# Kernel tuning notes

Hardware: AMD Instinct MI355X
Metric: run time of the kernel (lower is better)

Reference implementation:

```python
import math
import jax, jax.numpy as jnp
import numpy as np

B, S, D = 8, 512, 1024        # batch, seq (dec and enc), model dim
HID, NH = 1024, 16            # attention hidden, heads
C = HID // NH                 # per-head channels (self-attn 'attends' over this dim!)
EPS = 1e-5


def setup_inputs() -> dict:
    key = jax.random.key(0)
    ks = jax.random.split(key, 26)
    w = lambda k, sh: (jax.random.normal(k, sh, jnp.float32) * 0.02)
    inp = {
        "x": jax.random.normal(ks[0], (B, S, D), jnp.float32),
        "h": jax.random.normal(ks[1], (B, S, D), jnp.float32),
        # self-attn (AttentionModule) params, stored [in, out]
        "Wq": w(ks[2], (D, HID)), "bq": jnp.zeros((HID,), jnp.float32),
        "Wk": w(ks[3], (D, HID)), "bk": jnp.zeros((HID,), jnp.float32),
        "Wv": w(ks[4], (D, HID)), "bv": jnp.zeros((HID,), jnp.float32),
        "Wo": w(ks[5], (HID, D)), "bo": jnp.zeros((D,), jnp.float32),
        # cross-attn params
        "Wcq": w(ks[6], (D, HID)), "bcq": jnp.zeros((HID,), jnp.float32),
        "Wck": w(ks[7], (D, HID)), "bck": jnp.zeros((HID,), jnp.float32),
        "Wcv": w(ks[8], (D, HID)), "bcv": jnp.zeros((HID,), jnp.float32),
        "Wco": w(ks[9], (HID, D)), "bco": jnp.zeros((D,), jnp.float32),
        "gamma": jnp.ones((D,), jnp.float32), "beta": jnp.zeros((D,), jnp.float32),
        # FFN (two Linears, NO nonlinearity, per original code)
        "W1": w(ks[10], (D, HID)), "b1": jnp.zeros((HID,), jnp.float32),
        "W2": w(ks[11], (HID, D)), "b2": jnp.zeros((D,), jnp.float32),
    }
    return inp


def _layernorm(x, gamma, beta):
    mu = jnp.mean(x, axis=-1, keepdims=True)
    var = jnp.mean(jnp.square(x - mu), axis=-1, keepdims=True)
    return (x - mu) * jax.lax.rsqrt(var + EPS) * gamma + beta


def _self_attn(x, Wq, bq, Wk, bk, Wv, bv, Wo, bo):
    # FAITHFUL to original: reshape [B,S,NH,C]; einsum '...hq,...hk->...hqk' with
    # batch dims [B,S] -> attention over the C channel dim per token, causal mask over channels.
    Q = (x @ Wq + bq).reshape(B, S, NH, C) / math.sqrt(C)
    K = (x @ Wk + bk).reshape(B, S, NH, C)
    V = (x @ Wv + bv).reshape(B, S, NH, C)
    aff = jnp.einsum('bshq,bshk->bshqk', Q, K)            # [B,S,NH,C,C]
    mask = jnp.triu(jnp.full((C, C), -jnp.inf, jnp.float32), k=1)  # -inf above diag, 0 else
    aff = aff + mask
    w = jax.nn.softmax(aff, axis=-1)
    av = jnp.einsum('bshqk,bshk->bshq', w, V)             # [B,S,NH,C]
    return av.reshape(B, S, HID) @ Wo + bo


def _cross_attn(xd, he, Wcq, bcq, Wck, bck, Wcv, bcv, Wco, bco):
    # standard multi-head cross attention, but scaled by sqrt(d_full) per original
    Q = (xd @ Wcq + bcq).reshape(B, S, NH, C).transpose(0, 2, 1, 3)  # [B,NH,Sq,C]
    K = (he @ Wck + bck).reshape(B, S, NH, C).transpose(0, 2, 1, 3)
    V = (he @ Wcv + bcv).reshape(B, S, NH, C).transpose(0, 2, 1, 3)
    scores = jnp.einsum('bhqd,bhkd->bhqk', Q, K) / math.sqrt(HID)
    p = jax.nn.softmax(scores, axis=-1)
    o = jnp.einsum('bhqk,bhkd->bhqd', p, V)               # [B,NH,Sq,C]
    o = o.transpose(0, 2, 1, 3).reshape(B, S, HID)
    return o @ Wco + bco


def reference(x, h, Wq, bq, Wk, bk, Wv, bv, Wo, bo,
              Wcq, bcq, Wck, bck, Wcv, bcv, Wco, bco,
              gamma, beta, W1, b1, W2, b2):
    out = _self_attn(x, Wq, bq, Wk, bk, Wv, bv, Wo, bo) + x
    out = _layernorm(out, gamma, beta)
    out = _cross_attn(out, h, Wcq, bcq, Wck, bck, Wcv, bcv, Wco, bco) + out
    out = _layernorm(out, gamma, beta)
    out = ((out @ W1 + b1) @ W2 + b2) + out
    out = _layernorm(out, gamma, beta)
    return out
```

## Files before the change

### kernel.cpp

```cpp
#include <hip/hip_runtime.h>

typedef __bf16 bf16_t;
typedef bf16_t bf16x8 __attribute__((ext_vector_type(8)));
typedef bf16_t bf16x4 __attribute__((ext_vector_type(4)));
typedef float f32x4 __attribute__((ext_vector_type(4)));
typedef unsigned u32x4 __attribute__((ext_vector_type(4)));

__device__ __forceinline__ void async_copy16(const void* g, void* l) {
  __builtin_amdgcn_global_load_lds(
      (const __attribute__((address_space(1))) unsigned int*)(unsigned long long)g,
      (__attribute__((address_space(3))) unsigned int*)(unsigned int)(unsigned long long)l,
      16, 0, 0);
}

__device__ __forceinline__ float fast_exp2(float x) {
#if __has_builtin(__builtin_amdgcn_exp2f)
  return __builtin_amdgcn_exp2f(x);
#else
  float r;
  asm volatile("v_exp_f32 %0, %1\n\ts_nop 0" : "=v"(r) : "v"(x));
  return r;
#endif
}
__device__ __forceinline__ float fast_rcp(float x) {
#if __has_builtin(__builtin_amdgcn_rcpf)
  return __builtin_amdgcn_rcpf(x);
#else
  float r;
  asm volatile("v_rcp_f32 %0, %1\n\ts_nop 0" : "=v"(r) : "v"(x));
  return r;
#endif
}

__device__ __forceinline__ unsigned pack_bf16(float x, float y) {
  bf16_t lo = (bf16_t)x, hi = (bf16_t)y;
  unsigned short ul, uh;
  __builtin_memcpy(&ul, &lo, 2);
  __builtin_memcpy(&uh, &hi, 2);
  return (unsigned)ul | ((unsigned)uh << 16);
}

#define QSCALE 0.180336688f

struct SrcPtrs { const float* p[10]; };
__global__ __launch_bounds__(256) void prep_main(
    SrcPtrs srcs, bf16_t* __restrict__ dstbase,
    const float* __restrict__ a, const float* __restrict__ b,
    const float* __restrict__ w1, bf16_t* __restrict__ dst1,
    bf16_t* __restrict__ dstw) {
  __shared__ float tile[32][33];
  int bid = blockIdx.x;
  int tid = threadIdx.x;
  if (bid < 10240) {
    int z = bid >> 10;
    int rem = bid & 1023;
    const float* src = srcs.p[z];
    bf16_t* dst = dstbase + (size_t)z * 1048576;
    float scale = (z == 0) ? QSCALE : ((z == 4) ? 0.03125f : 1.f);
    int bx = (rem & 31) * 32;
    int by = (rem >> 5) * 32;
    int tx = tid & 31, ty = tid >> 5;
#pragma unroll
    for (int i = 0; i < 32; i += 8)
      tile[ty + i][tx] = src[(size_t)(by + ty + i) * 1024 + bx + tx];
    __syncthreads();
#pragma unroll
    for (int i = 0; i < 32; i += 8)
      dst[(size_t)(bx + ty + i) * 1024 + by + tx] = (bf16_t)(tile[tx][ty + i] * scale);
  } else {
    int i = ((bid - 10240) * 256 + tid) * 8;
    const float* s;
    bf16_t* d;
    if (i < 4194304) { s = a + i; d = dst1 + i; }
    else if (i < 8388608) { s = b + i - 4194304; d = dst1 + i; }
    else { s = w1 + i - 8388608; d = dstw + (i - 8388608); }
    float4 u = *(const float4*)s;
    float4 v = *(const float4*)(s + 4);
    bf16x8 o;
    o[0]=(bf16_t)u.x; o[1]=(bf16_t)u.y; o[2]=(bf16_t)u.z; o[3]=(bf16_t)u.w;
    o[4]=(bf16_t)v.x; o[5]=(bf16_t)v.y; o[6]=(bf16_t)v.z; o[7]=(bf16_t)v.w;
    *(bf16x8*)d = o;
  }
}

__global__ __launch_bounds__(256) void prep_bias_kernel(
    const float* __restrict__ bq, const float* __restrict__ bk,
    const float* __restrict__ bv, const float* __restrict__ bck,
    const float* __restrict__ bcv, const float* __restrict__ bcq,
    const bf16_t* __restrict__ wt9, const float* __restrict__ b1,
    const float* __restrict__ b2, float* __restrict__ cb,
    float* __restrict__ cb2) {
  int bid = blockIdx.x;
  if (bid < 28) {
    int i = bid * 256 + threadIdx.x;
    if (i < 1024) cb[i] = bq[i] * QSCALE;
    else if (i < 2048) cb[i] = bk[i - 1024];
    else if (i < 3072) cb[i] = bv[i - 2048];
    else if (i < 4096) cb[i] = bck[i - 3072];
    else if (i < 5120) cb[i] = bcv[i - 4096];
    else if (i < 6144) cb[i] = bcq[i - 5120] * 0.03125f;
    else cb[i] = 0.f;
  } else {
    int n = (bid - 28) * 256 + threadIdx.x;
    const bf16_t* row = wt9 + (size_t)n * 1024;
    float acc = 0.f;
#pragma unroll 4
    for (int h = 0; h < 1024; h += 8) {
      bf16x8 v = *(const bf16x8*)(row + h);
      float4 ba = *(const float4*)(b1 + h);
      float4 bb = *(const float4*)(b1 + h + 4);
      acc += ba.x*(float)v[0] + ba.y*(float)v[1] + ba.z*(float)v[2] + ba.w*(float)v[3]
           + bb.x*(float)v[4] + bb.y*(float)v[5] + bb.z*(float)v[6] + bb.w*(float)v[7];
    }
    cb2[n] = acc + b2[n];
  }
}

template <int BN, int MI, bool HAS_RES, bool TRANS_OUT, bool DBUF>
__device__ __forceinline__ void gemm_core(
    const bf16_t* __restrict__ A, const bf16_t* __restrict__ Bt,
    const float* __restrict__ bias, const bf16_t* __restrict__ res,
    bf16_t* __restrict__ C, int ldC, int bm, int bn,
    bf16_t* As, bf16_t* Bs) {
  constexpr int NI = 4;
  constexpr int ASZ = 128 * 64, BSZ = BN * 64;
  int tid = threadIdx.x;
  int w = tid >> 6, lane = tid & 63;
  int fm = lane & 15, fq = lane >> 4;
  int wm = (BN == 128) ? (w >> 1) * 64 : w * 32;
  int wn = (BN == 128) ? (w & 1) * 64 : 0;
  f32x4 acc[MI][NI] = {};

  auto stage = [&](int kt, int half) {
    bf16_t* Ad = DBUF ? As + half * ASZ : As;
    bf16_t* Bd = DBUF ? Bs + half * BSZ : Bs;
#pragma unroll
    for (int i = 0; i < 4; i++) {
      int c = i * 256 + tid;
      int row = c >> 3, skg = (c & 7) ^ (row & 7);
      async_copy16(A + (size_t)(bm + row) * 1024 + kt + skg * 8, &Ad[c * 8]);
    }
#pragma unroll
    for (int i = 0; i < BN / 32; i++) {
      int c = i * 256 + tid;
      int row = c >> 3, skg = (c & 7) ^ (row & 7);
      async_copy16(Bt + (size_t)(bn + row) * 1024 + kt + skg * 8, &Bd[c * 8]);
    }
  };
  auto compute = [&](int half) {
    const bf16_t* Ac = DBUF ? As + half * ASZ : As;
    const bf16_t* Bc = DBUF ? Bs + half * BSZ : Bs;
#pragma unroll
    for (int ks = 0; ks < 2; ks++) {
      bf16x8 af[MI], bfr[NI];
      int kg = ks * 4 + fq;
#pragma unroll
      for (int mi = 0; mi < MI; mi++) {
        int row = wm + mi * 16 + fm;
        af[mi] = *(const bf16x8*)&Ac[row * 64 + ((kg ^ (row & 7)) * 8)];
      }
#pragma unroll
      for (int ni = 0; ni < NI; ni++) {
        int row = wn + ni * 16 + fm;
        bfr[ni] = *(const bf16x8*)&Bc[row * 64 + ((kg ^ (row & 7)) * 8)];
      }
#pragma unroll
      for (int mi = 0; mi < MI; mi++)
#pragma unroll
        for (int ni = 0; ni < NI; ni++)
          acc[mi][ni] = __builtin_amdgcn_mfma_f32_16x16x32_bf16(
              af[mi], bfr[ni], acc[mi][ni], 0, 0, 0);
    }
  };

  if (DBUF) {
    stage(0, 0);
    __syncthreads();
#pragma unroll
    for (int t = 0; t < 16; t++) {
      if (t < 15) stage((t + 1) * 64, (t + 1) & 1);
      compute(t & 1);
      __syncthreads();
    }
  } else {
    for (int kt = 0; kt < 1024; kt += 64) {
      stage(kt, 0);
      __syncthreads();
      compute(0);
      __syncthreads();
    }
  }

#pragma unroll
  for (int mi = 0; mi < MI; mi++) {
#pragma unroll
    for (int ni = 0; ni < NI; ni++) {
      int col = bn + wn + ni * 16 + fm;
      float bv = bias[col];
      if (TRANS_OUT) {
        int rowb = bm + wm + mi * 16 + fq * 4;
        bf16x4 w4;
#pragma unroll
        for (int r = 0; r < 4; r++) w4[r] = (bf16_t)(acc[mi][ni][r] + bv);
        *(bf16x4*)&C[(size_t)col * ldC + rowb] = w4;
      } else {
#pragma unroll
        for (int r = 0; r < 4; r++) {
          int row = bm + wm + mi * 16 + fq * 4 + r;
          float v = acc[mi][ni][r] + bv;
          if (HAS_RES) v += (float)res[(size_t)row * ldC + col];
          C[(size_t)row * ldC + col] = (bf16_t)v;
        }
      }
    }
  }
}

template <int GX, int GY, int BN>
__device__ __forceinline__ void xcd_map(int lin, int& bm, int& bn) {
  constexpr int HX = GX / 2, QY = GY / 4;
  int xcd = lin & 7, idx = lin >> 3;
  int ly = idx / HX, lx = idx - ly * HX;
  bm = ((xcd >> 1) * QY + ly) * 128;
  bn = ((xcd & 1) * HX + lx) * BN;
}

template <bool HAS_RES, bool TRANS_OUT>
__global__ __launch_bounds__(256) void gemm_bf16(
    const bf16_t* __restrict__ A, const bf16_t* __restrict__ Bt,
    const float* __restrict__ bias, const bf16_t* __restrict__ res,
    bf16_t* __restrict__ C, int ldC) {
  __shared__ bf16_t As[2 * 128 * 64];
  __shared__ bf16_t Bs[2 * 64 * 64];
  int bm, bn;
  xcd_map<16, 32, 64>(blockIdx.x + 16 * blockIdx.y, bm, bn);
  gemm_core<64, 2, HAS_RES, TRANS_OUT, true>(A, Bt, bias, res, C, ldC, bm, bn, As, Bs);
}

__global__ __launch_bounds__(256) void gemm_qkv_p(
    const bf16_t* __restrict__ xb, const bf16_t* __restrict__ wt0,
    const bf16_t* __restrict__ wt9, const bf16_t* __restrict__ w1bf,
    const float* __restrict__ cb, bf16_t* __restrict__ qkv,
    bf16_t* __restrict__ pt) {
  __shared__ bf16_t smem[2 * 128 * 64];
  int bid = blockIdx.x;
  if (bid >= 128) {
    int bm, bn;
    xcd_map<24, 32, 128>(bid - 128, bm, bn);
    gemm_core<128, 4, false, false, false>(xb, wt0, cb, nullptr, qkv, 3072,
                                           bm, bn, smem, smem + 128 * 64);
  } else {
    gemm_core<64, 2, false, false, false>(wt9, w1bf, cb + 6144, nullptr, pt, 1024,
                                          (bid >> 4) * 128, (bid & 15) * 64,
                                          smem, smem + 128 * 64);
  }
}

__global__ __launch_bounds__(256) void gemm_cqkv(
    const bf16_t* __restrict__ t1n, const bf16_t* __restrict__ hb,
    const bf16_t* __restrict__ wt4, const float* __restrict__ cb,
    bf16_t* __restrict__ cq, bf16_t* __restrict__ kbuf,
    bf16_t* __restrict__ vt) {
  __shared__ bf16_t As[128 * 64];
  __shared__ bf16_t Bs[64 * 64];
  int lin = blockIdx.x + 48 * blockIdx.y;
  int xcd = lin & 7, idx = lin >> 3;
  int ly = idx / 24, lx = idx - ly * 24;
  int bm = ((xcd >> 1) * 8 + ly) * 128;
  int gx = (xcd & 1) * 24 + lx;
  int region = gx >> 4;
  int bn = (gx & 15) * 64;
  const bf16_t* Bt = wt4 + (size_t)region * 1048576;
  if (region == 2) {
    gemm_core<64, 2, false, true, false>(hb, Bt, cb + 4096, nullptr, vt, 4096,
                                         bm, bn, As, Bs);
  } else if (region == 1) {
    gemm_core<64, 2, false, false, false>(hb, Bt, cb + 3072, nullptr, kbuf, 1024,
                                          bm, bn, As, Bs);
  } else {
    gemm_core<64, 2, false, false, false>(t1n, Bt, cb + 5120, nullptr, cq, 1024,
                                          bm, bn, As, Bs);
  }
}

__global__ __launch_bounds__(256) void self_attn_kernel(
    const bf16_t* __restrict__ QKV, bf16_t* __restrict__ O) {
  int tid = threadIdx.x;
  int lane = tid & 63;
  int unit = __builtin_amdgcn_readfirstlane(blockIdx.x * 4 + (tid >> 6));
  int m = unit >> 4, h = unit & 15;
  size_t base = (size_t)m * 3072 + h * 64;
  size_t iq = base + lane;
  float qv = (float)QKV[iq];
  float kown = (float)QKV[iq + 1024];
  float vown = (float)QKV[iq + 2048];
  const u32x4* Krow = (const u32x4*)(QKV + base + 1024);
  const u32x4* Vrow = (const u32x4*)(QKV + base + 2048);
  u32x4 K4[8], V4[8];
#pragma unroll
  for (int i = 0; i < 8; i++) { K4[i] = Krow[i]; V4[i] = Vrow[i]; }
  float l0 = 0.f, l1 = 0.f, o0 = 0.f, o1 = 0.f;
#pragma unroll
  for (int p = 0; p < 32; p++) {
    unsigned kw = K4[p >> 2][p & 3];
    unsigned vw = V4[p >> 2][p & 3];
    float k0 = __uint_as_float(kw << 16);
    float k1 = __uint_as_float(kw & 0xffff0000u);
    float v0 = __uint_as_float(vw << 16);
    float v1 = __uint_as_float(vw & 0xffff0000u);
    float e0 = fast_exp2(qv * k0);
    float e1 = fast_exp2(qv * k1);
    bool c = lane >= 2 * p + 1;
    e0 = c ? e0 : 0.f;
    e1 = c ? e1 : 0.f;
    l0 += e0; o0 = fmaf(e0, v0, o0);
    l1 += e1; o1 = fmaf(e1, v1, o1);
  }
  float ed = fast_exp2(qv * kown);
  ed = ((lane & 1) == 0) ? ed : 0.f;
  float l = (l0 + l1) + ed;
  float o = fmaf(ed, vown, o0 + o1);
  O[(size_t)m * 1024 + h * 64 + lane] = (bf16_t)(o * fast_rcp(l));
}

__global__ __launch_bounds__(256) void cross_attn_mfma(
    const bf16_t* __restrict__ Q, const bf16_t* __restrict__ Kb,
    const bf16_t* __restrict__ Vt, bf16_t* __restrict__ O) {
  __shared__ bf16_t Ks[64 * 64];
  __shared__ bf16_t Vs[64 * 64];
  int tid = threadIdx.x;
  int w = tid >> 6, lane = tid & 63;
  int fm = lane & 15, fq = lane >> 4;
  int bh = blockIdx.x;
  int b = bh >> 4, h = bh & 15;
  int q0 = blockIdx.y * 64 + w * 16;
  const bf16_t* Qp = Q + (size_t)(b * 512 + q0 + fm) * 1024 + h * 64 + fq * 8;
  bf16x8 qf0 = *(const bf16x8*)Qp;
  bf16x8 qf1 = *(const bf16x8*)(Qp + 32);
  f32x4 o[4] = {};
  float mx = -1e30f, l = 0.f;
  for (int k0 = 0; k0 < 512; k0 += 64) {
    __syncthreads();
#pragma unroll
    for (int i = 0; i < 2; i++) {
      int c = i * 256 + tid;
      int row = c >> 3, kg = (c & 7) ^ (row & 7);
      async_copy16(Kb + (size_t)(b * 512 + k0 + row) * 1024 + h * 64 + kg * 8,
                   &Ks[c * 8]);
      async_copy16(Vt + (size_t)(h * 64 + row) * 4096 + b * 512 + k0 + kg * 8,
                   &Vs[c * 8]);
    }
    __syncthreads();
    f32x4 s[4] = {};
#pragma unroll
    for (int mt = 0; mt < 4; mt++) {
      int row = mt * 16 + fm;
#pragma unroll
      for (int f = 0; f < 2; f++) {
        int kg = f * 4 + fq;
        bf16x8 kf = *(const bf16x8*)&Ks[row * 64 + ((kg ^ (row & 7)) * 8)];
        s[mt] = __builtin_amdgcn_mfma_f32_16x16x32_bf16(
            kf, (f ? qf1 : qf0), s[mt], 0, 0, 0);
      }
    }
    float smax = -1e30f;
#pragma unroll
    for (int mt = 0; mt < 4; mt++)
#pragma unroll
      for (int r = 0; r < 4; r++) smax = fmaxf(smax, s[mt][r]);
    smax = fmaxf(smax, __shfl_xor(smax, 16, 64));
    smax = fmaxf(smax, __shfl_xor(smax, 32, 64));
    float nm = fmaxf(mx, smax);
    float corr = __expf(mx - nm);
    float ladd = 0.f;
    unsigned pk0[4], pk1[4];
#pragma unroll
    for (int mt = 0; mt < 4; mt++) {
      float p0 = __expf(s[mt][0] - nm);
      float p1 = __expf(s[mt][1] - nm);
      float p2 = __expf(s[mt][2] - nm);
      float p3 = __expf(s[mt][3] - nm);
      ladd += (p0 + p1) + (p2 + p3);
      pk0[mt] = pack_bf16(p0, p1);
      pk1[mt] = pack_bf16(p2, p3);
    }
    ladd += __shfl_xor(ladd, 16, 64);
    ladd += __shfl_xor(ladd, 32, 64);
    l = l * corr + ladd;
#pragma unroll
    for (int ct = 0; ct < 4; ct++)
#pragma unroll
      for (int r = 0; r < 4; r++) o[ct][r] *= corr;
    union U { unsigned u[4]; bf16x8 v; } pf[2];
    int sl0 = ((fq & 1) * 2) * 16 + fm;
    int sl1 = sl0 + 16;
    bool hi = fq >= 2;
#pragma unroll
    for (int f = 0; f < 2; f++) {
      unsigned a0 = (unsigned)__shfl((int)pk0[f * 2],     sl0, 64);
      unsigned b0 = (unsigned)__shfl((int)pk0[f * 2 + 1], sl0, 64);
      unsigned a1 = (unsigned)__shfl((int)pk1[f * 2],     sl0, 64);
      unsigned b1 = (unsigned)__shfl((int)pk1[f * 2 + 1], sl0, 64);
      unsigned a2 = (unsigned)__shfl((int)pk0[f * 2],     sl1, 64);
      unsigned b2 = (unsigned)__shfl((int)pk0[f * 2 + 1], sl1, 64);
      unsigned a3 = (unsigned)__shfl((int)pk1[f * 2],     sl1, 64);
      unsigned b3 = (unsigned)__shfl((int)pk1[f * 2 + 1], sl1, 64);
      pf[f].u[0] = hi ? b0 : a0;
      pf[f].u[1] = hi ? b1 : a1;
      pf[f].u[2] = hi ? b2 : a2;
      pf[f].u[3] = hi ? b3 : a3;
    }
#pragma unroll
    for (int ct = 0; ct < 4; ct++) {
      int row = ct * 16 + fm;
#pragma unroll
      for (int f = 0; f < 2; f++) {
        int kg = f * 4 + fq;
        bf16x8 vf = *(const bf16x8*)&Vs[row * 64 + ((kg ^ (row & 7)) * 8)];
        o[ct] = __builtin_amdgcn_mfma_f32_16x16x32_bf16(vf, pf[f].v, o[ct], 0, 0, 0);
      }
    }
    mx = nm;
  }
  float inv = 1.f / l;
  bf16_t* Op = O + (size_t)(b * 512 + q0 + fm) * 1024 + h * 64 + fq * 4;
#pragma unroll
  for (int ct = 0; ct < 4; ct++) {
    bf16x4 w4;
    w4[0] = (bf16_t)(o[ct][0] * inv);
    w4[1] = (bf16_t)(o[ct][1] * inv);
    w4[2] = (bf16_t)(o[ct][2] * inv);
    w4[3] = (bf16_t)(o[ct][3] * inv);
    *(bf16x4*)(Op + ct * 16) = w4;
  }
}

template <typename OutT>
__global__ __launch_bounds__(256) void ln_kernel(
    const bf16_t* __restrict__ X, const float* __restrict__ gamma,
    const float* __restrict__ beta, OutT* __restrict__ Y) {
  __shared__ float red[8];
  int row = blockIdx.x;
  int tid = threadIdx.x;
  bf16x4 x4 = *(const bf16x4*)(X + (size_t)row * 1024 + tid * 4);
  float4 v = {(float)x4[0], (float)x4[1], (float)x4[2], (float)x4[3]};
  float s = (v.x + v.y) + (v.z + v.w);
  float ss = fmaf(v.x, v.x, fmaf(v.y, v.y, fmaf(v.z, v.z, v.w * v.w)));
#pragma unroll
  for (int off = 32; off > 0; off >>= 1) {
    s  += __shfl_down(s, off, 64);
    ss += __shfl_down(ss, off, 64);
  }
  if ((tid & 63) == 0) { red[tid >> 6] = s; red[4 + (tid >> 6)] = ss; }
  __syncthreads();
  float S  = (red[0] + red[1]) + (red[2] + red[3]);
  float SS = (red[4] + red[5]) + (red[6] + red[7]);
  float mu = S * (1.f / 1024.f);
  float var = SS * (1.f / 1024.f) - mu * mu;
  float inv = rsqrtf(var + 1e-5f);
  float4 g = *(const float4*)(gamma + tid * 4);
  float4 b = *(const float4*)(beta + tid * 4);
  float r0 = (v.x - mu) * inv * g.x + b.x;
  float r1 = (v.y - mu) * inv * g.y + b.y;
  float r2 = (v.z - mu) * inv * g.z + b.z;
  float r3 = (v.w - mu) * inv * g.w + b.w;
  OutT* yp = Y + (size_t)row * 1024 + tid * 4;
  yp[0] = (OutT)r0; yp[1] = (OutT)r1; yp[2] = (OutT)r2; yp[3] = (OutT)r3;
}

extern "C" void kernel_launch(void* const* d_in, const int* in_sizes, int n_in,
                              void* d_out, int out_size, void* d_ws, size_t ws_size,
                              hipStream_t stream) {
  (void)in_sizes; (void)n_in; (void)out_size; (void)ws_size;
  const float* x  = (const float*)d_in[0];
  const float* hh = (const float*)d_in[1];
  SrcPtrs sp;
  sp.p[0] = (const float*)d_in[2];  sp.p[1] = (const float*)d_in[4];
  sp.p[2] = (const float*)d_in[6];  sp.p[3] = (const float*)d_in[8];
  sp.p[4] = (const float*)d_in[10]; sp.p[5] = (const float*)d_in[12];
  sp.p[6] = (const float*)d_in[14]; sp.p[7] = (const float*)d_in[16];
  sp.p[8] = (const float*)d_in[20]; sp.p[9] = (const float*)d_in[22];
  const float* W1f = (const float*)d_in[20];
  const float* bq  = (const float*)d_in[3];
  const float* bk  = (const float*)d_in[5];
  const float* bv  = (const float*)d_in[7];
  const float* bo  = (const float*)d_in[9];
  const float* bck = (const float*)d_in[13];
  const float* bcv = (const float*)d_in[15];
  const float* bcq = (const float*)d_in[11];
  const float* bco = (const float*)d_in[17];
  const float* gamma = (const float*)d_in[18];
  const float* beta  = (const float*)d_in[19];
  const float* b1  = (const float*)d_in[21];
  const float* b2  = (const float*)d_in[23];
  float* out = (float*)d_out;
  char* ws = (char*)d_ws;
  const size_t MB = 1048576;

  bf16_t* wt[10];
  for (int i = 0; i < 10; i++) wt[i] = (bf16_t*)(ws + (size_t)i * 2 * MB);
  float* cb      = (float*)(ws + 20 * MB);
  float* cb2     = (float*)(ws + 20 * MB + 32768);
  bf16_t* xb     = (bf16_t*)(ws + 21 * MB);
  bf16_t* hb     = (bf16_t*)(ws + 29 * MB);
  bf16_t* qkv    = (bf16_t*)(ws + 37 * MB);
  bf16_t* kbuf   = (bf16_t*)(ws + 37 * MB);
  bf16_t* vtbuf  = (bf16_t*)(ws + 45 * MB);
  bf16_t* cqbuf  = (bf16_t*)(ws + 61 * MB);
  bf16_t* attn   = (bf16_t*)(ws + 69 * MB);
  bf16_t* g4     = (bf16_t*)(ws + 77 * MB);
  bf16_t* ptbuf  = (bf16_t*)(ws + 85 * MB);
  bf16_t* w1bf   = (bf16_t*)(ws + 87 * MB);
  bf16_t* t1n    = xb;
  bf16_t* t2n    = hb;
  bf16_t* f2out  = g4;

  prep_main<<<14848, 256, 0, stream>>>(sp, (bf16_t*)ws, x, hh, W1f, xb, w1bf);
  prep_bias_kernel<<<32, 256, 0, stream>>>(bq, bk, bv, bck, bcv, bcq,
                                           wt[9], b1, b2, cb, cb2);

  gemm_qkv_p<<<896, 256, 0, stream>>>(xb, wt[0], wt[9], w1bf, cb, qkv, ptbuf);
  self_attn_kernel<<<16384, 256, 0, stream>>>(qkv, attn);
  gemm_bf16<true, false><<<dim3(16, 32), 256, 0, stream>>>(attn, wt[3], bo, xb, g4, 1024);
  ln_kernel<bf16_t><<<4096, 256, 0, stream>>>(g4, gamma, beta, t1n);
  gemm_cqkv<<<dim3(48, 32), 256, 0, stream>>>(t1n, hb, wt[4], cb, cqbuf, kbuf, vtbuf);
  cross_attn_mfma<<<dim3(128, 8), 256, 0, stream>>>(cqbuf, kbuf, vtbuf, attn);
  gemm_bf16<true, false><<<dim3(16, 32), 256, 0, stream>>>(attn, wt[7], bco, t1n, g4, 1024);
  ln_kernel<bf16_t><<<4096, 256, 0, stream>>>(g4, gamma, beta, t2n);
  gemm_bf16<true, false><<<dim3(16, 32), 256, 0, stream>>>(t2n, ptbuf, cb2, t2n, f2out, 1024);
  ln_kernel<float><<<4096, 256, 0, stream>>>(f2out, gamma, beta, out);
}
```

Before: 377.4 us.

## Fuse cross-attn K/V projection into self-attention launch to overlap work

The cross-attention K and V projections depend only on the encoder input h, so they move out of the post-LayerNorm cqkv GEMM into the self-attention launch as 1024 extra GEMM blocks. The memory-bound self-attention blocks then share the machine with compute-bound GEMM tiles, and the later cross-Q projection shrinks to a plain 1024-wide GEMM. Workspace buffers are reassigned so K/V no longer alias the QKV buffer that self-attention is still reading. The cost is a heterogeneous grid whose GEMM blocks may straggle or contend for resources with the attention blocks.

```diff
diff --git a/kernel.cpp b/kernel.cpp
--- a/kernel.cpp
+++ b/kernel.cpp
@@ -256,38 +256,33 @@
   }
 }
 
-__global__ __launch_bounds__(256) void gemm_cqkv(
-    const bf16_t* __restrict__ t1n, const bf16_t* __restrict__ hb,
-    const bf16_t* __restrict__ wt4, const float* __restrict__ cb,
-    bf16_t* __restrict__ cq, bf16_t* __restrict__ kbuf,
-    bf16_t* __restrict__ vt) {
+__global__ __launch_bounds__(256) void kvproj_selfattn(
+    const bf16_t* __restrict__ hb, const bf16_t* __restrict__ wt4,
+    const float* __restrict__ cb, bf16_t* __restrict__ kbuf,
+    bf16_t* __restrict__ vt, const bf16_t* __restrict__ QKV,
+    bf16_t* __restrict__ O) {
   __shared__ bf16_t As[128 * 64];
   __shared__ bf16_t Bs[64 * 64];
-  int lin = blockIdx.x + 48 * blockIdx.y;
-  int xcd = lin & 7, idx = lin >> 3;
-  int ly = idx / 24, lx = idx - ly * 24;
-  int bm = ((xcd >> 1) * 8 + ly) * 128;
-  int gx = (xcd & 1) * 24 + lx;
-  int region = gx >> 4;
-  int bn = (gx & 15) * 64;
-  const bf16_t* Bt = wt4 + (size_t)region * 1048576;
-  if (region == 2) {
-    gemm_core<64, 2, false, true, false>(hb, Bt, cb + 4096, nullptr, vt, 4096,
-                                         bm, bn, As, Bs);
-  } else if (region == 1) {
-    gemm_core<64, 2, false, false, false>(hb, Bt, cb + 3072, nullptr, kbuf, 1024,
-                                          bm, bn, As, Bs);
-  } else {
-    gemm_core<64, 2, false, false, false>(t1n, Bt, cb + 5120, nullptr, cq, 1024,
-                                          bm, bn, As, Bs);
-  }
-}
-
-__global__ __launch_bounds__(256) void self_attn_kernel(
-    const bf16_t* __restrict__ QKV, bf16_t* __restrict__ O) {
+  int bid = blockIdx.x;
+  if (bid < 1024) {
+    int xcd = bid & 7, idx = bid >> 3;
+    int ly = idx >> 4, lx = idx & 15;
+    int bm = ((xcd >> 1) * 8 + ly) * 128;
+    int region = 1 + (xcd & 1);
+    int bn = lx * 64;
+    const bf16_t* Bt = wt4 + (size_t)region * 1048576;
+    if (region == 2) {
+      gemm_core<64, 2, false, true, false>(hb, Bt, cb + 4096, nullptr, vt, 4096,
+                                           bm, bn, As, Bs);
+    } else {
+      gemm_core<64, 2, false, false, false>(hb, Bt, cb + 3072, nullptr, kbuf, 1024,
+                                            bm, bn, As, Bs);
+    }
+    return;
+  }
   int tid = threadIdx.x;
   int lane = tid & 63;
-  int unit = __builtin_amdgcn_readfirstlane(blockIdx.x * 4 + (tid >> 6));
+  int unit = __builtin_amdgcn_readfirstlane((bid - 1024) * 4 + (tid >> 6));
   int m = unit >> 4, h = unit & 15;
   size_t base = (size_t)m * 3072 + h * 64;
   size_t iq = base + lane;
@@ -504,11 +499,11 @@
   bf16_t* xb     = (bf16_t*)(ws + 21 * MB);
   bf16_t* hb     = (bf16_t*)(ws + 29 * MB);
   bf16_t* qkv    = (bf16_t*)(ws + 37 * MB);
-  bf16_t* kbuf   = (bf16_t*)(ws + 37 * MB);
-  bf16_t* vtbuf  = (bf16_t*)(ws + 45 * MB);
-  bf16_t* cqbuf  = (bf16_t*)(ws + 61 * MB);
-  bf16_t* attn   = (bf16_t*)(ws + 69 * MB);
-  bf16_t* g4     = (bf16_t*)(ws + 77 * MB);
+  bf16_t* cqbuf  = (bf16_t*)(ws + 37 * MB);
+  bf16_t* g4     = (bf16_t*)(ws + 45 * MB);
+  bf16_t* kbuf   = (bf16_t*)(ws + 61 * MB);
+  bf16_t* vtbuf  = (bf16_t*)(ws + 69 * MB);
+  bf16_t* attn   = (bf16_t*)(ws + 77 * MB);
   bf16_t* ptbuf  = (bf16_t*)(ws + 85 * MB);
   bf16_t* w1bf   = (bf16_t*)(ws + 87 * MB);
   bf16_t* t1n    = xb;
@@ -520,10 +515,11 @@
                                            wt[9], b1, b2, cb, cb2);
 
   gemm_qkv_p<<<896, 256, 0, stream>>>(xb, wt[0], wt[9], w1bf, cb, qkv, ptbuf);
-  self_attn_kernel<<<16384, 256, 0, stream>>>(qkv, attn);
+  kvproj_selfattn<<<17408, 256, 0, stream>>>(hb, wt[4], cb, kbuf, vtbuf, qkv, attn);
   gemm_bf16<true, false><<<dim3(16, 32), 256, 0, stream>>>(attn, wt[3], bo, xb, g4, 1024);
   ln_kernel<bf16_t><<<4096, 256, 0, stream>>>(g4, gamma, beta, t1n);
-  gemm_cqkv<<<dim3(48, 32), 256, 0, stream>>>(t1n, hb, wt[4], cb, cqbuf, kbuf, vtbuf);
+  gemm_bf16<false, false><<<dim3(16, 32), 256, 0, stream>>>(t1n, wt[4], cb + 5120,
+                                                            nullptr, cqbuf, 1024);
   cross_attn_mfma<<<dim3(128, 8), 256, 0, stream>>>(cqbuf, kbuf, vtbuf, attn);
   gemm_bf16<true, false><<<dim3(16, 32), 256, 0, stream>>>(attn, wt[7], bco, t1n, g4, 1024);
   ln_kernel<bf16_t><<<4096, 256, 0, stream>>>(g4, gamma, beta, t2n);
```

New measurement: 375.8 us. Within noise of the previous version (-0.4%).
